# Kernel tuning notes

Measured on AMD Instinct MI355X. Metric: run time of the kernel, lower is better.

## Reference

```python
import jax, jax.numpy as jnp
import numpy as np

NEG_INF = -10000000000.0
HEADS = 16


def setup_inputs() -> dict:
    key = jax.random.key(0)
    ks = jax.random.split(key, 12)
    B, S, E = 2, 2048, 1024
    sc = 1.0 / np.sqrt(E)
    inp = {
        "input_queries": jax.random.normal(ks[0], (B, S, E), jnp.float32),
        "input_keys": jax.random.normal(ks[1], (B, S, E), jnp.float32),
        "input_values": jax.random.normal(ks[2], (B, S, E), jnp.float32),
        # causal mask: True where attention is disallowed (masked_fill where mask==True)
        "mask": jnp.triu(jnp.ones((S, S), jnp.bool_), k=1)[None, None],
        "Wq": jax.random.normal(ks[3], (E, E), jnp.float32) * sc,
        "bq": jax.random.normal(ks[4], (E,), jnp.float32) * 0.01,
        "Wk": jax.random.normal(ks[5], (E, E), jnp.float32) * sc,
        "bk": jax.random.normal(ks[6], (E,), jnp.float32) * 0.01,
        "Wv": jax.random.normal(ks[7], (E, E), jnp.float32) * sc,
        "bv": jax.random.normal(ks[8], (E,), jnp.float32) * 0.01,
        "Wo": jax.random.normal(ks[9], (E, E), jnp.float32) * sc,
        "bo": jax.random.normal(ks[10], (E,), jnp.float32) * 0.01,
    }
    return inp


def reference(input_queries, input_keys, input_values, mask, Wq, bq, Wk, bk, Wv, bv, Wo, bo):
    B, S, E = input_queries.shape
    H = HEADS
    D = E // H
    # torch Linear: y = x @ W.T + b
    q = (input_queries @ Wq.T + bq).reshape(B, S, H, D).transpose(0, 2, 1, 3)  # bhsd
    k = (input_keys @ Wk.T + bk).reshape(B, S, H, D).transpose(0, 2, 1, 3)
    v = (input_values @ Wv.T + bv).reshape(B, S, H, D).transpose(0, 2, 1, 3)
    scores = jnp.einsum('bhqd,bhkd->bhqk', q, k) / jnp.sqrt(jnp.asarray(D, q.dtype))
    scores = jnp.where(mask, jnp.asarray(NEG_INF, scores.dtype), scores)
    attn = jax.nn.softmax(scores, axis=-1)
    out = jnp.einsum('bhqk,bhkd->bhqd', attn, v).transpose(0, 2, 1, 3).reshape(B, S, E)
    return out @ Wo.T + bo
```

## Files before the change

### kernel.cpp

```cpp
#include <hip/hip_runtime.h>
#include <hip/hip_bf16.h>

#define DEVI __device__ __forceinline__

using bf16x8 = __attribute__((ext_vector_type(8))) short;
using f32x4  = __attribute__((ext_vector_type(4))) float;
using f32x16 = __attribute__((ext_vector_type(16))) float;

#define LOG2E 1.4426950408889634f

DEVI unsigned short f2bf(float f){
  unsigned int u = __float_as_uint(f);
  return (unsigned short)((u + 0x7fffu + ((u>>16)&1u)) >> 16);
}

DEVI unsigned int cvt_pk_bf16(float lo, float hi){
  unsigned int r;
  asm("v_cvt_pk_bf16_f32 %0, %1, %2" : "=v"(r) : "v"(lo), "v"(hi));
  return r;
}

#if __has_builtin(__builtin_amdgcn_exp2f)
#define EXP2(x) __builtin_amdgcn_exp2f(x)
#else
#define EXP2(x) exp2f(x)
#endif

DEVI void gload_lds16(const unsigned short* src, unsigned short* lds){
  __builtin_amdgcn_global_load_lds((const __attribute__((address_space(1))) void*)src,
                                   (__attribute__((address_space(3))) void*)lds, 16, 0, 0);
}

DEVI bf16x8 mk8(unsigned w0, unsigned w1, unsigned w2, unsigned w3){
  union { unsigned u[4]; bf16x8 v; } x;
  x.u[0]=w0; x.u[1]=w1; x.u[2]=w2; x.u[3]=w3;
  return x.v;
}

__global__ __launch_bounds__(256) void convert_kernel(
  const float* __restrict__ Xq, const float* __restrict__ Xk, const float* __restrict__ Xv,
  const float* __restrict__ Wq, const float* __restrict__ Wk, const float* __restrict__ Wv,
  const float* __restrict__ Wo, unsigned short* __restrict__ ws)
{
  const int y = blockIdx.y;
  const float* src;
  unsigned short* dst;
  int n4;
  if (y < 3){
    src = (y==0)?Xq:((y==1)?Xk:Xv);
    dst = ws + (size_t)y*4194304;
    n4 = 1048576;
  } else {
    src = (y==3)?Wq:((y==4)?Wk:((y==5)?Wv:Wo));
    dst = ws + 12582912 + (size_t)(y-3)*1048576;
    n4 = 262144;
  }
  const int stride = gridDim.x * 256;
  for (int i = blockIdx.x*256 + threadIdx.x; i < n4; i += stride){
    float4 v = ((const float4*)src)[i];
    uint2 u;
    u.x = cvt_pk_bf16(v.x, v.y);
    u.y = cvt_pk_bf16(v.z, v.w);
    ((uint2*)dst)[i] = u;
  }
}

__global__ __launch_bounds__(256) void proj_qkv_kernel(
  const unsigned short* __restrict__ Xb, const unsigned short* __restrict__ Wb,
  const float* __restrict__ Bq, const float* __restrict__ Bk, const float* __restrict__ Bv,
  unsigned short* __restrict__ Qo, unsigned short* __restrict__ Ko, unsigned short* __restrict__ Vo)
{
  const int L = blockIdx.x;
  const int xcd = L & 7, g = L >> 3;
  const int combo = xcd*12 + (g>>3);
  const int tn = g & 7;
  const int p  = combo >> 5;
  const int tm = combo & 31;

  const unsigned short* __restrict__ A = Xb + (size_t)p*4194304;
  const unsigned short* __restrict__ B = Wb + (size_t)p*1048576;
  const float* __restrict__ Bb = (p==0)?Bq:((p==1)?Bk:Bv);
  unsigned short* __restrict__ Out = (p==0)?Qo:((p==1)?Ko:Vo);
  const float oscale = (p==0)?(0.125f*LOG2E):1.0f;

  const int m0 = tm*128, n0 = tn*128;
  const int tid = threadIdx.x;
  const int w = tid>>6, l = tid&63;
  const int wr = w>>1, wc = w&1;
  const int lg = l>>4, lr = l&15;

  __shared__ unsigned short As[2][8192];
  __shared__ unsigned short Bs[2][8192];

  f32x4 acc[4][4];
  #pragma unroll
  for (int i=0;i<4;i++)
    #pragma unroll
    for (int j=0;j<4;j++){ f32x4 z = {0.f,0.f,0.f,0.f}; acc[i][j] = z; }

  const int sub = l>>3;
  const int kc  = (l&7) ^ sub;
  auto stage = [&](int kt, int h){
    #pragma unroll
    for (int i=0;i<4;i++){
      int rbase = w*32 + i*8;
      gload_lds16(A + (size_t)(m0+rbase+sub)*1024 + kt + kc*8, &As[h][0] + rbase*64);
      gload_lds16(B + (size_t)(n0+rbase+sub)*1024 + kt + kc*8, &Bs[h][0] + rbase*64);
    }
  };

  stage(0, 0);
  asm volatile("s_waitcnt vmcnt(0)" ::: "memory");
  __builtin_amdgcn_s_barrier();

  int cur = 0;
  for (int kt6=0; kt6<16; kt6++){
    if (kt6 < 15) stage((kt6+1)*64, cur^1);

    #pragma unroll
    for (int ck=0;ck<2;ck++){
      bf16x8 af[4], bfr[4];
      #pragma unroll
      for (int f=0;f<4;f++){
        int ra = wr*64 + f*16 + lr;
        af[f]  = *(const bf16x8*)((const char*)&As[cur][0] + ra*128 + ((ck*64 + lg*16) ^ ((ra&7)<<4)));
        int rb = wc*64 + f*16 + lr;
        bfr[f] = *(const bf16x8*)((const char*)&Bs[cur][0] + rb*128 + ((ck*64 + lg*16) ^ ((rb&7)<<4)));
      }
      #pragma unroll
      for (int fr=0;fr<4;fr++)
        #pragma unroll
        for (int fc=0;fc<4;fc++)
          acc[fr][fc] = __builtin_amdgcn_mfma_f32_16x16x32_bf16(af[fr], bfr[fc], acc[fr][fc], 0,0,0);
    }

    asm volatile("s_waitcnt vmcnt(0)" ::: "memory");
    __builtin_amdgcn_s_barrier();
    cur ^= 1;
  }

  if (p == 2){
    #pragma unroll
    for (int fc=0;fc<4;fc++){
      int n = n0 + wc*64 + fc*16 + lr;
      float bias = Bb[n];
      int h = n>>6, d = n&63;
      #pragma unroll
      for (int fr=0;fr<4;fr++){
        int m = m0 + wr*64 + fr*16 + lg*4;
        int b = m>>11, s = m & 2047;
        uint2 u;
        u.x = cvt_pk_bf16(acc[fr][fc][0]+bias, acc[fr][fc][1]+bias);
        u.y = cvt_pk_bf16(acc[fr][fc][2]+bias, acc[fr][fc][3]+bias);
        *(uint2*)(Out + (((size_t)((b<<4)+h)*64 + d)*2048 + s)) = u;
      }
    }
  } else {
    #pragma unroll
    for (int fc=0;fc<4;fc++){
      int n = n0 + wc*64 + fc*16 + lr;
      float bias = Bb[n];
      int h = n>>6, d = n&63;
      #pragma unroll
      for (int fr=0;fr<4;fr++){
        #pragma unroll
        for (int r=0;r<4;r++){
          int m = m0 + wr*64 + fr*16 + lg*4 + r;
          int b = m>>11, s = m & 2047;
          float v = (acc[fr][fc][r] + bias) * oscale;
          Out[ ((size_t)((b<<4)+h)*2048 + (size_t)s)*64 + d ] = f2bf(v);
        }
      }
    }
  }
}

__global__ __launch_bounds__(256,2) void attn_kernel(
  const unsigned short* __restrict__ Q, const unsigned short* __restrict__ Kg,
  const unsigned short* __restrict__ Vt, unsigned short* __restrict__ AO)
{
  const int idx = blockIdx.x;
  const int qt = 15 - (idx >> 5);
  const int bh = idx & 31;
  const size_t base = (size_t)bh * 131072;
  const int q0 = qt * 128;
  const int tid = threadIdx.x, w = tid>>6, l = tid&63;
  const int lq = l & 31, hi = l >> 5;
  const int qq = q0 + w*32 + lq;

  __shared__ unsigned short Ks[2][4096];
  __shared__ unsigned short Vs[2][4096];

  bf16x8 qf[4];
  {
    const unsigned short* qp = Q + base + (size_t)qq*64;
    #pragma unroll
    for (int s=0;s<4;s++) qf[s] = *(const bf16x8*)(qp + s*16 + hi*8);
  }

  f32x16 oacc[2];
  #pragma unroll
  for (int dt=0;dt<2;dt++)
    #pragma unroll
    for (int r=0;r<16;r++) oacc[dt][r] = 0.f;
  float m_i = -INFINITY, l_i = 0.f;

  const int NT = 2*qt + 2;

  auto stage = [&](int kt, int half){
    const int kv0 = kt*64;
    #pragma unroll
    for (int i=0;i<2;i++){
      int c = tid + i*256;
      int row = c>>3;
      int kc = (c&7) ^ (row&7);
      gload_lds16(Kg + base + (size_t)(kv0+row)*64 + kc*8, &Ks[half][0] + c*8);
      gload_lds16(Vt + base + (size_t)row*2048 + kv0 + kc*8, &Vs[half][0] + c*8);
    }
  };

  stage(0, 0);
  __syncthreads();

  for (int kt=0; kt<NT; kt++){
    const int cur = kt & 1;
    if (kt+1 < NT) stage(kt+1, cur^1);
    const int kv0 = kt*64;

    f32x16 sacc[2];
    #pragma unroll
    for (int kvt=0;kvt<2;kvt++)
      #pragma unroll
      for (int r=0;r<16;r++) sacc[kvt][r] = 0.f;

    __builtin_amdgcn_s_setprio(1);
    #pragma unroll
    for (int kvt=0;kvt<2;kvt++){
      int row = kvt*32 + lq;
      const char* kb = (const char*)&Ks[cur][0] + row*128;
      int swz = (row&7)<<4;
      #pragma unroll
      for (int s=0;s<4;s++){
        bf16x8 kf = *(const bf16x8*)(kb + ((s*32 + hi*16) ^ swz));
        sacc[kvt] = __builtin_amdgcn_mfma_f32_32x32x16_bf16(kf, qf[s], sacc[kvt], 0,0,0);
      }
    }
    __builtin_amdgcn_s_setprio(0);

    #pragma unroll
    for (int kvt=0;kvt<2;kvt++){
      if (kv0 + kvt*32 + 31 > q0 + w*32){
        #pragma unroll
        for (int r=0;r<16;r++){
          int kvv = kv0 + kvt*32 + (r&3) + 8*(r>>2) + 4*hi;
          if (kvv > qq) sacc[kvt][r] = -1e30f;
        }
      }
    }

    float mt = sacc[0][0];
    #pragma unroll
    for (int kvt=0;kvt<2;kvt++)
      #pragma unroll
      for (int r=0;r<16;r++) mt = fmaxf(mt, sacc[kvt][r]);
    mt = fmaxf(mt, __shfl_xor(mt, 32));

    if (__any(mt > m_i + 8.f)){
      float mn = fmaxf(m_i, mt);
      float sc = EXP2(m_i - mn);
      m_i = mn;
      l_i *= sc;
      #pragma unroll
      for (int dt=0;dt<2;dt++)
        #pragma unroll
        for (int r=0;r<16;r++) oacc[dt][r] *= sc;
    }
    float rs = 0.f;
    #pragma unroll
    for (int kvt=0;kvt<2;kvt++)
      #pragma unroll
      for (int r=0;r<16;r++){
        float pv = EXP2(sacc[kvt][r] - m_i);
        sacc[kvt][r] = pv;
        rs += pv;
      }
    rs += __shfl_xor(rs, 32);
    l_i += rs;

    unsigned pa[8], pb[8], sa[8], sb[8];
    #pragma unroll
    for (int g=0; g<8; g++){
      int kvt = g>>2, gl = g&3;
      pa[g] = cvt_pk_bf16(sacc[kvt][4*gl+0], sacc[kvt][4*gl+1]);
      pb[g] = cvt_pk_bf16(sacc[kvt][4*gl+2], sacc[kvt][4*gl+3]);
      sa[g] = __shfl_xor(pa[g], 32);
      sb[g] = __shfl_xor(pb[g], 32);
    }
    bf16x8 pfrag[4];
    #pragma unroll
    for (int s=0;s<4;s++){
      int g0 = (s>>1)*4 + 2*(s&1);
      unsigned w0 = hi ? sa[g0+1] : pa[g0];
      unsigned w1 = hi ? sb[g0+1] : pb[g0];
      unsigned w2 = hi ? pa[g0+1] : sa[g0];
      unsigned w3 = hi ? pb[g0+1] : sb[g0];
      pfrag[s] = mk8(w0, w1, w2, w3);
    }

    __builtin_amdgcn_s_setprio(1);
    #pragma unroll
    for (int dt=0;dt<2;dt++){
      int row = dt*32 + lq;
      const char* vb = (const char*)&Vs[cur][0] + row*128;
      int swz = (row&7)<<4;
      #pragma unroll
      for (int s=0;s<4;s++){
        bf16x8 vf = *(const bf16x8*)(vb + ((s*32 + hi*16) ^ swz));
        oacc[dt] = __builtin_amdgcn_mfma_f32_32x32x16_bf16(vf, pfrag[s], oacc[dt], 0,0,0);
      }
    }
    __builtin_amdgcn_s_setprio(0);

    __syncthreads();
  }

  unsigned short* Es = &Ks[0][0] + w*2048;
  float inv = 1.0f / l_i;
  {
    char* eb = (char*)Es + lq*128;
    int swz = (lq&7)<<4;
    #pragma unroll
    for (int dt=0;dt<2;dt++)
      #pragma unroll
      for (int g=0;g<4;g++){
        int d0 = dt*32 + 8*g + 4*hi;
        unsigned u0 = cvt_pk_bf16(oacc[dt][4*g+0]*inv, oacc[dt][4*g+1]*inv);
        unsigned u1 = cvt_pk_bf16(oacc[dt][4*g+2]*inv, oacc[dt][4*g+3]*inv);
        *(unsigned*)(eb + ((d0*2    ) ^ swz)) = u0;
        *(unsigned*)(eb + ((d0*2 + 4) ^ swz)) = u1;
      }
  }
  const int b = bh>>4, h = bh&15;
  {
    const char* rb = (const char*)Es + lq*128;
    int swz = (lq&7)<<4;
    unsigned short* op = AO + ((size_t)b*2048 + (q0 + w*32 + lq))*1024 + h*64 + hi*32;
    #pragma unroll
    for (int j=0;j<2;j++){
      bf16x8 v = *(const bf16x8*)(rb + ((hi*64 + j*16) ^ swz));
      *(bf16x8*)(op + j*8) = v;
    }
    #pragma unroll
    for (int j=2;j<4;j++){
      bf16x8 v = *(const bf16x8*)(rb + ((hi*64 + j*16) ^ swz));
      *(bf16x8*)(op + j*8) = v;
    }
  }
}

__global__ __launch_bounds__(256) void proj_out_kernel(
  const unsigned short* __restrict__ A, const unsigned short* __restrict__ B,
  const float* __restrict__ Bb, float* __restrict__ Out)
{
  const int L = blockIdx.x;
  const int xcd = L & 7, g = L >> 3;
  const int tm = xcd*4 + (g>>3);
  const int tn = g & 7;
  const int m0 = tm*128, n0 = tn*128;
  const int tid = threadIdx.x;
  const int w = tid>>6, l = tid&63;
  const int wr = w>>1, wc = w&1;
  const int lg = l>>4, lr = l&15;

  __shared__ unsigned short As[2][8192];
  __shared__ unsigned short Bs[2][8192];

  f32x4 acc[4][4];
  #pragma unroll
  for (int i=0;i<4;i++)
    #pragma unroll
    for (int j=0;j<4;j++){ f32x4 z = {0.f,0.f,0.f,0.f}; acc[i][j] = z; }

  const int sub = l>>3;
  const int kc  = (l&7) ^ sub;
  auto stage = [&](int kt, int h){
    #pragma unroll
    for (int i=0;i<4;i++){
      int rbase = w*32 + i*8;
      gload_lds16(A + (size_t)(m0+rbase+sub)*1024 + kt + kc*8, &As[h][0] + rbase*64);
      gload_lds16(B + (size_t)(n0+rbase+sub)*1024 + kt + kc*8, &Bs[h][0] + rbase*64);
    }
  };

  stage(0, 0);
  asm volatile("s_waitcnt vmcnt(0)" ::: "memory");
  __builtin_amdgcn_s_barrier();

  int cur = 0;
  for (int kt6=0; kt6<16; kt6++){
    if (kt6 < 15) stage((kt6+1)*64, cur^1);

    #pragma unroll
    for (int ck=0;ck<2;ck++){
      bf16x8 af[4], bfr[4];
      #pragma unroll
      for (int f=0;f<4;f++){
        int ra = wr*64 + f*16 + lr;
        af[f]  = *(const bf16x8*)((const char*)&As[cur][0] + ra*128 + ((ck*64 + lg*16) ^ ((ra&7)<<4)));
        int rb = wc*64 + f*16 + lr;
        bfr[f] = *(const bf16x8*)((const char*)&Bs[cur][0] + rb*128 + ((ck*64 + lg*16) ^ ((rb&7)<<4)));
      }
      #pragma unroll
      for (int fr=0;fr<4;fr++)
        #pragma unroll
        for (int fc=0;fc<4;fc++)
          acc[fr][fc] = __builtin_amdgcn_mfma_f32_16x16x32_bf16(af[fr], bfr[fc], acc[fr][fc], 0,0,0);
    }

    asm volatile("s_waitcnt vmcnt(0)" ::: "memory");
    __builtin_amdgcn_s_barrier();
    cur ^= 1;
  }

  #pragma unroll
  for (int fc=0;fc<4;fc++){
    int n = n0 + wc*64 + fc*16 + lr;
    float bias = Bb[n];
    #pragma unroll
    for (int fr=0;fr<4;fr++){
      #pragma unroll
      for (int r=0;r<4;r++){
        int m = m0 + wr*64 + fr*16 + lg*4 + r;
        Out[(size_t)m*1024 + n] = acc[fr][fc][r] + bias;
      }
    }
  }
}

extern "C" void kernel_launch(void* const* d_in, const int* in_sizes, int n_in,
                              void* d_out, int out_size, void* d_ws, size_t ws_size,
                              hipStream_t stream)
{
  const float* Xq = (const float*)d_in[0];
  const float* Xk = (const float*)d_in[1];
  const float* Xv = (const float*)d_in[2];
  const float* Wq = (const float*)d_in[4];
  const float* bq = (const float*)d_in[5];
  const float* Wk = (const float*)d_in[6];
  const float* bk = (const float*)d_in[7];
  const float* Wv = (const float*)d_in[8];
  const float* bv = (const float*)d_in[9];
  const float* Wo = (const float*)d_in[10];
  const float* bo = (const float*)d_in[11];

  unsigned short* ws  = (unsigned short*)d_ws;
  unsigned short* Xb  = ws;
  unsigned short* Wb  = ws + 12582912;
  unsigned short* Qw  = ws + 16777216;
  unsigned short* Kw  = ws + 20971520;
  unsigned short* Vw  = ws + 25165824;
  unsigned short* AOw = ws + 29360128;
  float* out = (float*)d_out;

  convert_kernel<<<dim3(512,7), 256, 0, stream>>>(Xq,Xk,Xv,Wq,Wk,Wv,Wo, ws);
  proj_qkv_kernel<<<768, 256, 0, stream>>>(Xb, Wb, bq,bk,bv, Qw,Kw,Vw);
  attn_kernel<<<512, 256, 0, stream>>>(Qw,Kw,Vw,AOw);
  proj_out_kernel<<<256, 256, 0, stream>>>(AOw, Wb + 3*1048576, bo, out);
}
```

Measured before the change: 249.2 us.

## Switch projection GEMMs to triple-buffered K=32 stages with partial vmcnt waits

Both projection GEMM kernels move from a double-buffered K=64 LDS pipeline to a triple-buffered K=32 pipeline. Loads for two stages ahead are in flight, and each iteration waits with vmcnt(4) rather than draining all loads, so global-to-LDS copies overlap more with MFMA work. LDS per block drops from 64KB to 48KB, with a new XOR swizzle for 64-byte rows, and launch bounds request 3 blocks per CU for more occupancy. The cost is twice as many barriers per K and smaller MFMA batches per barrier.

Result: faster. 235.5 us (-5.5%).

```diff
diff --git a/kernel.cpp b/kernel.cpp
--- a/kernel.cpp
+++ b/kernel.cpp
@@ -65,7 +65,7 @@
   }
 }
 
-__global__ __launch_bounds__(256) void proj_qkv_kernel(
+__global__ __launch_bounds__(256, 3) void proj_qkv_kernel(
   const unsigned short* __restrict__ Xb, const unsigned short* __restrict__ Wb,
   const float* __restrict__ Bq, const float* __restrict__ Bk, const float* __restrict__ Bv,
   unsigned short* __restrict__ Qo, unsigned short* __restrict__ Ko, unsigned short* __restrict__ Vo)
@@ -89,8 +89,8 @@
   const int wr = w>>1, wc = w&1;
   const int lg = l>>4, lr = l&15;
 
-  __shared__ unsigned short As[2][8192];
-  __shared__ unsigned short Bs[2][8192];
+  __shared__ unsigned short As[3][4096];
+  __shared__ unsigned short Bs[3][4096];
 
   f32x4 acc[4][4];
   #pragma unroll
@@ -98,45 +98,46 @@
     #pragma unroll
     for (int j=0;j<4;j++){ f32x4 z = {0.f,0.f,0.f,0.f}; acc[i][j] = z; }
 
-  const int sub = l>>3;
-  const int kc  = (l&7) ^ sub;
-  auto stage = [&](int kt, int h){
-    #pragma unroll
-    for (int i=0;i<4;i++){
-      int rbase = w*32 + i*8;
-      gload_lds16(A + (size_t)(m0+rbase+sub)*1024 + kt + kc*8, &As[h][0] + rbase*64);
-      gload_lds16(B + (size_t)(n0+rbase+sub)*1024 + kt + kc*8, &Bs[h][0] + rbase*64);
+  const int srow = l>>2;
+  const int schk = (l&3) ^ (srow&3);
+  auto stage = [&](int h, int buf){
+    const int kt = h*32;
+    #pragma unroll
+    for (int i=0;i<2;i++){
+      int rbase = w*32 + i*16;
+      gload_lds16(A + (size_t)(m0+rbase+srow)*1024 + kt + schk*8, &As[buf][0] + rbase*32);
+      gload_lds16(B + (size_t)(n0+rbase+srow)*1024 + kt + schk*8, &Bs[buf][0] + rbase*32);
     }
   };
 
   stage(0, 0);
-  asm volatile("s_waitcnt vmcnt(0)" ::: "memory");
-  __builtin_amdgcn_s_barrier();
-
+  stage(1, 1);
+
+  const int sca = (lg ^ (lr&3)) << 4;
   int cur = 0;
-  for (int kt6=0; kt6<16; kt6++){
-    if (kt6 < 15) stage((kt6+1)*64, cur^1);
-
-    #pragma unroll
-    for (int ck=0;ck<2;ck++){
-      bf16x8 af[4], bfr[4];
-      #pragma unroll
-      for (int f=0;f<4;f++){
-        int ra = wr*64 + f*16 + lr;
-        af[f]  = *(const bf16x8*)((const char*)&As[cur][0] + ra*128 + ((ck*64 + lg*16) ^ ((ra&7)<<4)));
-        int rb = wc*64 + f*16 + lr;
-        bfr[f] = *(const bf16x8*)((const char*)&Bs[cur][0] + rb*128 + ((ck*64 + lg*16) ^ ((rb&7)<<4)));
-      }
-      #pragma unroll
-      for (int fr=0;fr<4;fr++)
-        #pragma unroll
-        for (int fc=0;fc<4;fc++)
-          acc[fr][fc] = __builtin_amdgcn_mfma_f32_16x16x32_bf16(af[fr], bfr[fc], acc[fr][fc], 0,0,0);
-    }
-
-    asm volatile("s_waitcnt vmcnt(0)" ::: "memory");
+  for (int h=0; h<32; ++h){
+    if (h < 31) asm volatile("s_waitcnt vmcnt(4)" ::: "memory");
+    else        asm volatile("s_waitcnt vmcnt(0)" ::: "memory");
     __builtin_amdgcn_s_barrier();
-    cur ^= 1;
+    __builtin_amdgcn_sched_barrier(0);
+    if (h < 30){
+      int nb = cur + 2; if (nb >= 3) nb -= 3;
+      stage(h+2, nb);
+    }
+
+    bf16x8 af[4], bfr[4];
+    #pragma unroll
+    for (int f=0;f<4;f++){
+      af[f]  = *(const bf16x8*)((const char*)&As[cur][0] + (wr*64 + f*16 + lr)*64 + sca);
+      bfr[f] = *(const bf16x8*)((const char*)&Bs[cur][0] + (wc*64 + f*16 + lr)*64 + sca);
+    }
+    #pragma unroll
+    for (int fr=0;fr<4;fr++)
+      #pragma unroll
+      for (int fc=0;fc<4;fc++)
+        acc[fr][fc] = __builtin_amdgcn_mfma_f32_16x16x32_bf16(af[fr], bfr[fc], acc[fr][fc], 0,0,0);
+
+    cur = (cur==2) ? 0 : cur+1;
   }
 
   if (p == 2){
@@ -358,7 +359,7 @@
   }
 }
 
-__global__ __launch_bounds__(256) void proj_out_kernel(
+__global__ __launch_bounds__(256, 3) void proj_out_kernel(
   const unsigned short* __restrict__ A, const unsigned short* __restrict__ B,
   const float* __restrict__ Bb, float* __restrict__ Out)
 {
@@ -372,8 +373,8 @@
   const int wr = w>>1, wc = w&1;
   const int lg = l>>4, lr = l&15;
 
-  __shared__ unsigned short As[2][8192];
-  __shared__ unsigned short Bs[2][8192];
+  __shared__ unsigned short As[3][4096];
+  __shared__ unsigned short Bs[3][4096];
 
   f32x4 acc[4][4];
   #pragma unroll
@@ -381,45 +382,46 @@
     #pragma unroll
     for (int j=0;j<4;j++){ f32x4 z = {0.f,0.f,0.f,0.f}; acc[i][j] = z; }
 
-  const int sub = l>>3;
-  const int kc  = (l&7) ^ sub;
-  auto stage = [&](int kt, int h){
-    #pragma unroll
-    for (int i=0;i<4;i++){
-      int rbase = w*32 + i*8;
-      gload_lds16(A + (size_t)(m0+rbase+sub)*1024 + kt + kc*8, &As[h][0] + rbase*64);
-      gload_lds16(B + (size_t)(n0+rbase+sub)*1024 + kt + kc*8, &Bs[h][0] + rbase*64);
+  const int srow = l>>2;
+  const int schk = (l&3) ^ (srow&3);
+  auto stage = [&](int h, int buf){
+    const int kt = h*32;
+    #pragma unroll
+    for (int i=0;i<2;i++){
+      int rbase = w*32 + i*16;
+      gload_lds16(A + (size_t)(m0+rbase+srow)*1024 + kt + schk*8, &As[buf][0] + rbase*32);
+      gload_lds16(B + (size_t)(n0+rbase+srow)*1024 + kt + schk*8, &Bs[buf][0] + rbase*32);
     }
   };
 
   stage(0, 0);
-  asm volatile("s_waitcnt vmcnt(0)" ::: "memory");
-  __builtin_amdgcn_s_barrier();
-
+  stage(1, 1);
+
+  const int sca = (lg ^ (lr&3)) << 4;
   int cur = 0;
-  for (int kt6=0; kt6<16; kt6++){
-    if (kt6 < 15) stage((kt6+1)*64, cur^1);
-
-    #pragma unroll
-    for (int ck=0;ck<2;ck++){
-      bf16x8 af[4], bfr[4];
-      #pragma unroll
-      for (int f=0;f<4;f++){
-        int ra = wr*64 + f*16 + lr;
-        af[f]  = *(const bf16x8*)((const char*)&As[cur][0] + ra*128 + ((ck*64 + lg*16) ^ ((ra&7)<<4)));
-        int rb = wc*64 + f*16 + lr;
-        bfr[f] = *(const bf16x8*)((const char*)&Bs[cur][0] + rb*128 + ((ck*64 + lg*16) ^ ((rb&7)<<4)));
-      }
-      #pragma unroll
-      for (int fr=0;fr<4;fr++)
-        #pragma unroll
-        for (int fc=0;fc<4;fc++)
-          acc[fr][fc] = __builtin_amdgcn_mfma_f32_16x16x32_bf16(af[fr], bfr[fc], acc[fr][fc], 0,0,0);
-    }
-
-    asm volatile("s_waitcnt vmcnt(0)" ::: "memory");
+  for (int h=0; h<32; ++h){
+    if (h < 31) asm volatile("s_waitcnt vmcnt(4)" ::: "memory");
+    else        asm volatile("s_waitcnt vmcnt(0)" ::: "memory");
     __builtin_amdgcn_s_barrier();
-    cur ^= 1;
+    __builtin_amdgcn_sched_barrier(0);
+    if (h < 30){
+      int nb = cur + 2; if (nb >= 3) nb -= 3;
+      stage(h+2, nb);
+    }
+
+    bf16x8 af[4], bfr[4];
+    #pragma unroll
+    for (int f=0;f<4;f++){
+      af[f]  = *(const bf16x8*)((const char*)&As[cur][0] + (wr*64 + f*16 + lr)*64 + sca);
+      bfr[f] = *(const bf16x8*)((const char*)&Bs[cur][0] + (wc*64 + f*16 + lr)*64 + sca);
+    }
+    #pragma unroll
+    for (int fr=0;fr<4;fr++)
+      #pragma unroll
+      for (int fc=0;fc<4;fc++)
+        acc[fr][fc] = __builtin_amdgcn_mfma_f32_16x16x32_bf16(af[fr], bfr[fc], acc[fr][fc], 0,0,0);
+
+    cur = (cur==2) ? 0 : cur+1;
   }
 
   #pragma unroll
```
